# Performance work log

Measured on AMD Instinct MI355X. Metric: run time of the kernel, lower is better.

## Reference

```python
import jax, jax.numpy as jnp
import numpy as np

EMBED = 1024
HEADS = 16
HEAD_DIM = EMBED // HEADS
NUM_BUCKETS = 32
MAX_DISTANCE = 128
B, L = 4, 2048


def relative_position_bucket(relative_position, num_buckets=NUM_BUCKETS, max_distance=MAX_DISTANCE):
    # Faithful port of the torch helper (unidirectional T5 bucketing).
    n = -relative_position                       # [L, L] int32
    max_exact = num_buckets // 2
    is_small = n < max_exact
    nf = jnp.maximum(n, 1).astype(jnp.float32)   # guard log(<=0); masked out by is_small
    val_if_large = max_exact + (
        jnp.log(nf / max_exact) / np.log(max_distance / max_exact) * (num_buckets - max_exact)
    ).astype(jnp.int32)                          # .long() in torch truncates; values >=0 here
    val_if_large = jnp.minimum(val_if_large, num_buckets - 1)
    ret = jnp.where(is_small, n, val_if_large)
    return jnp.maximum(ret, 0)


def setup_inputs() -> dict:
    key = jax.random.key(0)
    ks = jax.random.split(key, 11)
    s = 0.02
    return {
        "x": jax.random.normal(ks[0], (B, L, EMBED), dtype=jnp.float32),
        "wq": jax.random.normal(ks[1], (EMBED, EMBED), dtype=jnp.float32) * s,
        "bq": jnp.zeros((EMBED,), dtype=jnp.float32),
        "wk": jax.random.normal(ks[2], (EMBED, EMBED), dtype=jnp.float32) * s,
        "bk": jnp.zeros((EMBED,), dtype=jnp.float32),
        "wv": jax.random.normal(ks[3], (EMBED, EMBED), dtype=jnp.float32) * s,
        "bv": jnp.zeros((EMBED,), dtype=jnp.float32),
        "wo": jax.random.normal(ks[4], (EMBED, EMBED), dtype=jnp.float32) * s,
        "bo": jnp.zeros((EMBED,), dtype=jnp.float32),
        "rel_bias": jax.random.normal(ks[5], (NUM_BUCKETS, HEADS), dtype=jnp.float32) * s,
    }


def reference(x, wq, bq, wk, bk, wv, bv, wo, bo, rel_bias):
    Bx, Lx, C = x.shape
    # torch nn.Linear: y = x @ W.T + b
    def proj(w, b):
        y = jnp.einsum("blc,dc->bld", x, w) + b
        return y.reshape(Bx, Lx, HEADS, HEAD_DIM).transpose(0, 2, 1, 3)  # [B,H,L,Dh]
    q = proj(wq, bq)
    k = proj(wk, bk)
    v = proj(wv, bv)
    scores = jnp.einsum("bhqd,bhkd->bhqk", q, k) / np.sqrt(HEAD_DIM)  # [B,H,L,L]
    ctx = jnp.arange(Lx, dtype=jnp.int32)
    relative = ctx[None, :] - ctx[:, None]                            # [L,L]
    bucket_ids = relative_position_bucket(relative)                   # [L,L]
    bias = rel_bias[bucket_ids]                                       # [L,L,H]
    bias = jnp.transpose(bias, (2, 0, 1))                             # [H,L,L]
    attn = jax.nn.softmax(scores + bias[None], axis=-1)
    out = jnp.einsum("bhqk,bhkd->bhqd", attn, v)                      # [B,H,L,Dh]
    out = out.transpose(0, 2, 1, 3).reshape(Bx, Lx, C)
    return jnp.einsum("blc,dc->bld", out, wo) + bo
```

## Files before the change

kernel.cpp:

```cpp
#include <hip/hip_runtime.h>

typedef __bf16 bf16x8 __attribute__((ext_vector_type(8)));
typedef __bf16 bf16x2 __attribute__((ext_vector_type(2)));
typedef float f32x4 __attribute__((ext_vector_type(4)));
typedef float f32x16 __attribute__((ext_vector_type(16)));
typedef short short8v __attribute__((ext_vector_type(8)));
typedef unsigned uint4v __attribute__((ext_vector_type(4)));
typedef unsigned short ushort_t;

#define EMB 1024
#define HEADS 16
#define HDIM 64
#define BATCH 4
#define SEQ 2048
#define LOG2E 1.44269504088896340736f
#define FIXED_M 12.0f

__device__ __forceinline__ ushort_t f2bf(float f) {
  union { float f; unsigned u; } x; x.f = f;
  unsigned r = x.u + 0x7fffu + ((x.u >> 16) & 1u);
  return (ushort_t)(r >> 16);
}

__device__ __forceinline__ unsigned pack2(float lo, float hi) {
  bf16x2 t;
  t.x = (__bf16)lo;
  t.y = (__bf16)hi;
  return __builtin_bit_cast(unsigned, t);
}

__device__ __forceinline__ void gload_lds16(const void* g, void* l) {
  __builtin_amdgcn_global_load_lds(
      (const __attribute__((address_space(1))) void*)g,
      (__attribute__((address_space(3))) void*)l, 16, 0, 0);
}

__global__ __launch_bounds__(256) void convert_all(
    const float* __restrict__ x,
    const float* __restrict__ wq, const float* __restrict__ wk,
    const float* __restrict__ wv, const float* __restrict__ wo,
    ushort_t* __restrict__ xb, ushort_t* __restrict__ wqb,
    ushort_t* __restrict__ wkb, ushort_t* __restrict__ wvb,
    ushort_t* __restrict__ wob) {
  int cid = blockIdx.x * 256 + threadIdx.x;
  const float* src;
  ushort_t* dst;
  int off;
  if (cid < 1048576) {
    src = x; dst = xb; off = cid;
  } else {
    int r = cid - 1048576;
    int wi = r >> 17;
    off = r & 131071;
    src = wi == 0 ? wq : wi == 1 ? wk : wi == 2 ? wv : wo;
    dst = wi == 0 ? wqb : wi == 1 ? wkb : wi == 2 ? wvb : wob;
  }
  const float4* s4 = (const float4*)(src + (size_t)off * 8);
  float4 a = s4[0], b = s4[1];
  ushort_t tmp[8] = {f2bf(a.x), f2bf(a.y), f2bf(a.z), f2bf(a.w),
                     f2bf(b.x), f2bf(b.y), f2bf(b.z), f2bf(b.w)};
  *(short8v*)(dst + (size_t)off * 8) = *(const short8v*)tmp;
}

__global__ __launch_bounds__(256) void build_biasR(
    const float* __restrict__ rel_bias, float* __restrict__ biasR) {
  int fid = blockIdx.x * 256 + threadIdx.x;
  int hh = fid >> 12;
  int p = (fid >> 10) & 3;
  int j = fid & 1023;
#pragma unroll
  for (int e = 0; e < 4; ++e) {
    int r = 4 * j + p + e;
    int n = 2048 - r;
    int bucket;
    if (n < 16) {
      bucket = n > 0 ? n : 0;
    } else {
      float tt = logf((float)n * 0.0625f) * (16.0f / logf(8.0f));
      int v = 16 + (int)tt;
      bucket = v < 31 ? v : 31;
    }
    biasR[(size_t)fid * 4 + e] = rel_bias[bucket * HEADS + hh] * LOG2E - FIXED_M;
  }
}

__global__ __launch_bounds__(256) void gemm_qkv(
    const ushort_t* __restrict__ xb,
    const ushort_t* __restrict__ wqb, const ushort_t* __restrict__ wkb,
    const ushort_t* __restrict__ wvb,
    const float* __restrict__ bq, const float* __restrict__ bk,
    const float* __restrict__ bv,
    ushort_t* __restrict__ qb, ushort_t* __restrict__ kb,
    ushort_t* __restrict__ vtb) {
  const int wgid = blockIdx.x;
  const int xcd = wgid & 7;
  const int r0 = wgid >> 3;
  const int nb = r0 % 24;
  const int mb = (r0 / 24) * 8 + xcd;
  const int wsel = nb >> 3;
  const int nloc = (nb & 7) * 128;
  const ushort_t* W = wsel == 0 ? wqb : wsel == 1 ? wkb : wvb;
  const float* bias = wsel == 0 ? bq : wsel == 1 ? bk : bv;
  const float scale = wsel == 0 ? 0.125f * LOG2E : 1.0f;

  __shared__ ushort_t Al[128 * 64];
  __shared__ ushort_t Bl[128 * 64];
  const int tid = threadIdx.x, lane = tid & 63, wid = tid >> 6;
  const int wm = wid >> 1, wn = wid & 1;
  const int srow = lane >> 3;
  const int scol = (lane & 7) * 8;
  f32x4 acc[4][4] = {};

  for (int kt = 0; kt < EMB / 64; ++kt) {
    const int k0 = kt * 64;
#pragma unroll
    for (int i = 0; i < 4; ++i) {
      int c = i * 4 + wid;
      int row = c * 8 + srow;
      gload_lds16(xb + (size_t)(mb * 128 + row) * EMB + k0 + scol, &Al[c * 512]);
      gload_lds16(W + (size_t)(nloc + row) * EMB + k0 + scol, &Bl[c * 512]);
    }
    __syncthreads();
#pragma unroll
    for (int kk = 0; kk < 2; ++kk) {
      const int koff = kk * 32 + (lane >> 4) * 8;
      bf16x8 af[4], bfv[4];
#pragma unroll
      for (int m = 0; m < 4; ++m)
        af[m] = *(const bf16x8*)&Al[(wm * 64 + m * 16 + (lane & 15)) * 64 + koff];
#pragma unroll
      for (int n = 0; n < 4; ++n)
        bfv[n] = *(const bf16x8*)&Bl[(wn * 64 + n * 16 + (lane & 15)) * 64 + koff];
#pragma unroll
      for (int m = 0; m < 4; ++m)
#pragma unroll
        for (int n = 0; n < 4; ++n)
          acc[m][n] = __builtin_amdgcn_mfma_f32_16x16x32_bf16(af[m], bfv[n],
                                                              acc[m][n], 0, 0, 0);
    }
    __syncthreads();
  }

#pragma unroll
  for (int m = 0; m < 4; ++m)
#pragma unroll
    for (int n = 0; n < 4; ++n)
#pragma unroll
      for (int r = 0; r < 4; ++r) {
        int row = mb * 128 + wm * 64 + m * 16 + (lane >> 4) * 4 + r;
        int col = nloc + wn * 64 + n * 16 + (lane & 15);
        float v = (acc[m][n][r] + bias[col]) * scale;
        int b = row >> 11, l = row & 2047;
        int hh = col >> 6, d = col & 63;
        if (wsel == 2) {
          vtb[(((size_t)(b * HEADS + hh) * HDIM) + d) * SEQ + l] = f2bf(v);
        } else {
          ushort_t* outp = wsel == 0 ? qb : kb;
          outp[(((size_t)(b * HEADS + hh) * SEQ) + l) * HDIM + d] = f2bf(v);
        }
      }
}

__global__ __launch_bounds__(256) void gemm_out(
    const ushort_t* __restrict__ ctxb, const ushort_t* __restrict__ wob,
    const float* __restrict__ bo, float* __restrict__ out) {
  const int wgid = blockIdx.x;
  const int xcd = wgid & 7;
  const int r0 = wgid >> 3;
  const int nb = r0 & 7;
  const int mb = (r0 >> 3) * 8 + xcd;
  __shared__ ushort_t Al[128 * 64];
  __shared__ ushort_t Bl[128 * 64];
  const int tid = threadIdx.x, lane = tid & 63, wid = tid >> 6;
  const int wm = wid >> 1, wn = wid & 1;
  const int srow = lane >> 3;
  const int scol = (lane & 7) * 8;
  f32x4 acc[4][4] = {};

  for (int kt = 0; kt < EMB / 64; ++kt) {
    const int k0 = kt * 64;
#pragma unroll
    for (int i = 0; i < 4; ++i) {
      int c = i * 4 + wid;
      int row = c * 8 + srow;
      gload_lds16(ctxb + (size_t)(mb * 128 + row) * EMB + k0 + scol, &Al[c * 512]);
      gload_lds16(wob + (size_t)(nb * 128 + row) * EMB + k0 + scol, &Bl[c * 512]);
    }
    __syncthreads();
#pragma unroll
    for (int kk = 0; kk < 2; ++kk) {
      const int koff = kk * 32 + (lane >> 4) * 8;
      bf16x8 af[4], bfv[4];
#pragma unroll
      for (int m = 0; m < 4; ++m)
        af[m] = *(const bf16x8*)&Al[(wm * 64 + m * 16 + (lane & 15)) * 64 + koff];
#pragma unroll
      for (int n = 0; n < 4; ++n)
        bfv[n] = *(const bf16x8*)&Bl[(wn * 64 + n * 16 + (lane & 15)) * 64 + koff];
#pragma unroll
      for (int m = 0; m < 4; ++m)
#pragma unroll
        for (int n = 0; n < 4; ++n)
          acc[m][n] = __builtin_amdgcn_mfma_f32_16x16x32_bf16(af[m], bfv[n],
                                                              acc[m][n], 0, 0, 0);
    }
    __syncthreads();
  }

#pragma unroll
  for (int m = 0; m < 4; ++m)
#pragma unroll
    for (int n = 0; n < 4; ++n)
#pragma unroll
      for (int r = 0; r < 4; ++r) {
        int row = mb * 128 + wm * 64 + m * 16 + (lane >> 4) * 4 + r;
        int col = nb * 128 + wn * 64 + n * 16 + (lane & 15);
        out[(size_t)row * EMB + col] = acc[m][n][r] + bo[col];
      }
}

__global__ __launch_bounds__(256) void attn(
    const ushort_t* __restrict__ qb, const ushort_t* __restrict__ kb,
    const ushort_t* __restrict__ vtb, const float* __restrict__ biasR,
    ushort_t* __restrict__ ctxb) {
  const int wgid = blockIdx.x;
  const int xcd = wgid & 7;
  const int sidx = wgid >> 3;
  const int qblk = sidx & 15;
  const int bh = ((sidx >> 4) << 3) | xcd;
  const int h = bh & 15, b = bh >> 4;
  const int tid = threadIdx.x;
  const int lane = tid & 63, w = tid >> 6;
  const int l31 = lane & 31, hi5 = lane >> 5;
  const int pidx = (lane ^ 32) << 2;

  __shared__ ushort_t SM[16384];

  const size_t base = (size_t)bh * (SEQ * HDIM);
  const int q = qblk * 128 + w * 32 + l31;

  bf16x8 qf[4];
#pragma unroll
  for (int s = 0; s < 4; ++s)
    qf[s] = *(const bf16x8*)&qb[base + (size_t)q * HDIM + s * 16 + hi5 * 8];

  int koA[4];
#pragma unroll
  for (int s = 0; s < 4; ++s)
    koA[s] = (s * 16 + hi5 * 8) ^ ((l31 & 7) << 3);
  const int rb0 = l31 * 64;
  const int rb1 = rb0 + 2048;

  const int p = (4 - (q & 3)) & 3;
  const int j00 = ((4 * hi5 - q + 2048) - p) >> 2;
  const float4* bptr = (const float4*)biasR + ((h * 4 + p) * 1024 + j00);

  const int chR0 = tid >> 3, chC0 = (tid & 7) * 8;
  const int chR1 = chR0 + 32;
  const int kd0 = chR0 * 64 + (chC0 ^ ((chR0 & 7) << 3));
  const int kd1 = chR1 * 64 + (chC0 ^ ((chR1 & 7) << 3));

  const ushort_t* kp0 = kb + base + (size_t)chR0 * HDIM + chC0;
  const ushort_t* kp1 = kb + base + (size_t)chR1 * HDIM + chC0;
  const ushort_t* vp0 = vtb + base + (size_t)chR0 * SEQ + chC0;
  const ushort_t* vp1 = vtb + base + (size_t)chR1 * SEQ + chC0;

  short8v kr0 = *(const short8v*)kp0;
  short8v kr1 = *(const short8v*)kp1;
  short8v vr0 = *(const short8v*)vp0;
  short8v vr1 = *(const short8v*)vp1;
  *(short8v*)&SM[kd0] = kr0;
  *(short8v*)&SM[kd1] = kr1;
  *(short8v*)&SM[4096 + kd0] = vr0;
  *(short8v*)&SM[4096 + kd1] = vr1;
  kp0 += 64 * HDIM; kp1 += 64 * HDIM; vp0 += 64; vp1 += 64;
  kr0 = *(const short8v*)kp0;
  kr1 = *(const short8v*)kp1;
  vr0 = *(const short8v*)vp0;
  vr1 = *(const short8v*)vp1;
  __syncthreads();

  f32x16 o0 = {}, o1 = {}, lv = {};

#pragma unroll 2
  for (int t = 0; t < 32; ++t) {
    const int c = t & 1;
    ushort_t* Kl = SM + c * 8192;
    ushort_t* Vl = Kl + 4096;

    float4 bw[8];
#pragma unroll
    for (int hh = 0; hh < 2; ++hh)
#pragma unroll
      for (int g = 0; g < 4; ++g)
        bw[hh * 4 + g] = bptr[hh * 8 + g * 2];

    f32x16 s0 = {}, s1 = {};
    __builtin_amdgcn_s_setprio(1);
#pragma unroll
    for (int s = 0; s < 4; ++s) {
      bf16x8 ka = *(const bf16x8*)&Kl[rb0 + koA[s]];
      s0 = __builtin_amdgcn_mfma_f32_32x32x16_bf16(ka, qf[s], s0, 0, 0, 0);
    }
#pragma unroll
    for (int s = 0; s < 4; ++s) {
      bf16x8 ka = *(const bf16x8*)&Kl[rb1 + koA[s]];
      s1 = __builtin_amdgcn_mfma_f32_32x32x16_bf16(ka, qf[s], s1, 0, 0, 0);
    }
    __builtin_amdgcn_s_setprio(0);

    if (t < 31) {
      ushort_t* Kn = SM + (c ^ 1) * 8192;
      *(short8v*)&Kn[kd0] = kr0;
      *(short8v*)&Kn[kd1] = kr1;
      *(short8v*)&Kn[4096 + kd0] = vr0;
      *(short8v*)&Kn[4096 + kd1] = vr1;
      kp0 += 64 * HDIM; kp1 += 64 * HDIM; vp0 += 64; vp1 += 64;
      kr0 = *(const short8v*)kp0;
      kr1 = *(const short8v*)kp1;
      vr0 = *(const short8v*)vp0;
      vr1 = *(const short8v*)vp1;
    }

#pragma unroll
    for (int r = 0; r < 16; ++r) {
      s0[r] += bw[r >> 2][r & 3];
      s1[r] += bw[4 + (r >> 2)][r & 3];
    }
#pragma unroll
    for (int r = 0; r < 16; ++r) s0[r] = __builtin_amdgcn_exp2f(s0[r]);
#pragma unroll
    for (int r = 0; r < 16; ++r) s1[r] = __builtin_amdgcn_exp2f(s1[r]);
    lv += s0;
    lv += s1;

    unsigned pk0[8], pk1[8];
#pragma unroll
    for (int d = 0; d < 8; ++d) {
      pk0[d] = pack2(s0[2 * d], s0[2 * d + 1]);
      pk1[d] = pack2(s1[2 * d], s1[2 * d + 1]);
    }
#pragma unroll
    for (int gsel = 0; gsel < 4; ++gsel) {
      int a = (gsel & 1) + (gsel >> 1) * 4;
      int bqi = a + 2;
      {
        unsigned tmp = hi5 ? pk0[a] : pk0[bqi];
        unsigned got = (unsigned)__builtin_amdgcn_ds_bpermute(pidx, (int)tmp);
        pk0[bqi] = hi5 ? pk0[bqi] : got;
        pk0[a] = hi5 ? got : pk0[a];
      }
      {
        unsigned tmp = hi5 ? pk1[a] : pk1[bqi];
        unsigned got = (unsigned)__builtin_amdgcn_ds_bpermute(pidx, (int)tmp);
        pk1[bqi] = hi5 ? pk1[bqi] : got;
        pk1[a] = hi5 ? got : pk1[a];
      }
    }

    bf16x8 paf[4];
    {
      uint4v t0 = {pk0[0], pk0[1], pk0[2], pk0[3]};
      uint4v t1 = {pk0[4], pk0[5], pk0[6], pk0[7]};
      uint4v t2 = {pk1[0], pk1[1], pk1[2], pk1[3]};
      uint4v t3 = {pk1[4], pk1[5], pk1[6], pk1[7]};
      paf[0] = __builtin_bit_cast(bf16x8, t0);
      paf[1] = __builtin_bit_cast(bf16x8, t1);
      paf[2] = __builtin_bit_cast(bf16x8, t2);
      paf[3] = __builtin_bit_cast(bf16x8, t3);
    }

    __builtin_amdgcn_s_setprio(1);
#pragma unroll
    for (int ss = 0; ss < 4; ++ss) {
      bf16x8 vb0 = *(const bf16x8*)&Vl[rb0 + koA[ss]];
      bf16x8 vb1 = *(const bf16x8*)&Vl[rb1 + koA[ss]];
      o0 = __builtin_amdgcn_mfma_f32_32x32x16_bf16(paf[ss], vb0, o0, 0, 0, 0);
      o1 = __builtin_amdgcn_mfma_f32_32x32x16_bf16(paf[ss], vb1, o1, 0, 0, 0);
    }
    __builtin_amdgcn_s_setprio(0);

    if (t < 31) __syncthreads();
    bptr += 16;
  }

  float li = (((lv[0] + lv[1]) + (lv[2] + lv[3])) +
              ((lv[4] + lv[5]) + (lv[6] + lv[7]))) +
             (((lv[8] + lv[9]) + (lv[10] + lv[11])) +
              ((lv[12] + lv[13]) + (lv[14] + lv[15])));
  float li2 = __int_as_float(
      __builtin_amdgcn_ds_bpermute(pidx, __float_as_int(li)));
  li += li2;
  float inv = 1.0f / li;
#pragma unroll
  for (int r = 0; r < 16; ++r) {
    int qr = (r & 3) + 8 * (r >> 2) + 4 * hi5;
    float iv = __int_as_float(
        __builtin_amdgcn_ds_bpermute(qr << 2, __float_as_int(inv)));
    o0[r] *= iv;
    o1[r] *= iv;
  }
  ushort_t* T = SM + w * 2048;
#pragma unroll
  for (int r = 0; r < 16; ++r) {
    int qr = (r & 3) + 8 * (r >> 2) + 4 * hi5;
    int sw = (qr & 7) << 3;
    T[qr * 64 + (l31 ^ sw)] = f2bf(o0[r]);
    T[qr * 64 + ((32 + l31) ^ sw)] = f2bf(o1[r]);
  }
  const int qr2 = lane >> 1;
  const int dh0 = (lane & 1) * 32;
  const int sw2 = (qr2 & 7) << 3;
  const size_t crow =
      ((size_t)b * SEQ + qblk * 128 + w * 32 + qr2) * EMB + h * 64;
#pragma unroll
  for (int c = 0; c < 4; ++c) {
    short8v vv = *(const short8v*)&T[qr2 * 64 + ((dh0 + c * 8) ^ sw2)];
    *(short8v*)&ctxb[crow + dh0 + c * 8] = vv;
  }
}

extern "C" void kernel_launch(void* const* d_in, const int* in_sizes, int n_in,
                              void* d_out, int out_size, void* d_ws, size_t ws_size,
                              hipStream_t stream) {
  const float* x = (const float*)d_in[0];
  const float* wq = (const float*)d_in[1];
  const float* bq = (const float*)d_in[2];
  const float* wk = (const float*)d_in[3];
  const float* bk = (const float*)d_in[4];
  const float* wv = (const float*)d_in[5];
  const float* bv = (const float*)d_in[6];
  const float* wo = (const float*)d_in[7];
  const float* bo = (const float*)d_in[8];
  const float* rel_bias = (const float*)d_in[9];
  float* out = (float*)d_out;

  char* ws = (char*)d_ws;
  ushort_t* xb  = (ushort_t*)(ws);
  ushort_t* wqb = (ushort_t*)(ws + 16777216);
  ushort_t* wkb = (ushort_t*)(ws + 16777216 + 2097152);
  ushort_t* wvb = (ushort_t*)(ws + 16777216 + 2 * 2097152);
  ushort_t* wob = (ushort_t*)(ws + 16777216 + 3 * 2097152);
  ushort_t* qb  = (ushort_t*)(ws + 25165824);
  ushort_t* kb  = (ushort_t*)(ws + 25165824 + 16777216);
  ushort_t* vtb = (ushort_t*)(ws + 25165824 + 2 * 16777216);
  float* biasR  = (float*)(ws + 75497472);
  ushort_t* ctxb = xb;

  convert_all<<<6144, 256, 0, stream>>>(x, wq, wk, wv, wo, xb, wqb, wkb, wvb, wob);
  build_biasR<<<256, 256, 0, stream>>>(rel_bias, biasR);
  gemm_qkv<<<1536, 256, 0, stream>>>(xb, wqb, wkb, wvb, bq, bk, bv, qb, kb, vtb);
  attn<<<1024, 256, 0, stream>>>(qb, kb, vtb, biasR, ctxb);
  gemm_out<<<512, 256, 0, stream>>>(ctxb, wob, bo, out);
}
```

Before: 283.7 us.

## Read K directly from global and stream V into LDS with direct loads

The attention kernel now uses 128-thread blocks covering 64 queries each, launched as 2048 blocks with a launch-bounds occupancy hint. K fragments are loaded straight from global memory into registers instead of being staged through shared memory. V tiles are double-buffered in LDS via direct global-to-LDS loads, synchronised by a single raw barrier plus a vmcnt wait. This removes the register-staged K/V copies and half the LDS footprint, at the cost of redundant per-wave K reads from cache and fragile hand-tuned wait counts.

```diff
diff --git a/kernel.cpp b/kernel.cpp
--- a/kernel.cpp
+++ b/kernel.cpp
@@ -219,30 +219,47 @@
       }
 }
 
-__global__ __launch_bounds__(256) void attn(
+__global__ __launch_bounds__(128, 4) void attn(
     const ushort_t* __restrict__ qb, const ushort_t* __restrict__ kb,
     const ushort_t* __restrict__ vtb, const float* __restrict__ biasR,
     ushort_t* __restrict__ ctxb) {
   const int wgid = blockIdx.x;
   const int xcd = wgid & 7;
   const int sidx = wgid >> 3;
-  const int qblk = sidx & 15;
-  const int bh = ((sidx >> 4) << 3) | xcd;
+  const int qblk = sidx & 31;
+  const int bh = ((sidx >> 5) << 3) | xcd;
   const int h = bh & 15, b = bh >> 4;
   const int tid = threadIdx.x;
   const int lane = tid & 63, w = tid >> 6;
   const int l31 = lane & 31, hi5 = lane >> 5;
   const int pidx = (lane ^ 32) << 2;
 
-  __shared__ ushort_t SM[16384];
+  __shared__ ushort_t SM[8192];
 
   const size_t base = (size_t)bh * (SEQ * HDIM);
-  const int q = qblk * 128 + w * 32 + l31;
+  const int q0 = qblk * 64 + w * 32;
+  const int q = q0 + l31;
 
   bf16x8 qf[4];
 #pragma unroll
   for (int s = 0; s < 4; ++s)
     qf[s] = *(const bf16x8*)&qb[base + (size_t)q * HDIM + s * 16 + hi5 * 8];
+
+  const ushort_t* kpA = kb + base + (size_t)l31 * HDIM + hi5 * 8;
+  const ushort_t* kpB = kpA + 32 * HDIM;
+
+  const int p = (4 - (q & 3)) & 3;
+  const int j00 = ((4 * hi5 - q + 2048) - p) >> 2;
+  const float4* bptr = (const float4*)biasR + ((h * 4 + p) * 1024 + j00);
+
+  const int vrow = w * 32 + (lane >> 3);
+  const ushort_t* vsrc =
+      vtb + base + (size_t)vrow * SEQ + ((lane & 7) ^ (lane >> 3)) * 8;
+  const int vdst = (w * 32) * 64;
+
+#pragma unroll
+  for (int i = 0; i < 4; ++i)
+    gload_lds16(vsrc + (size_t)i * 8 * SEQ, SM + vdst + i * 512);
 
   int koA[4];
 #pragma unroll
@@ -251,43 +268,9 @@
   const int rb0 = l31 * 64;
   const int rb1 = rb0 + 2048;
 
-  const int p = (4 - (q & 3)) & 3;
-  const int j00 = ((4 * hi5 - q + 2048) - p) >> 2;
-  const float4* bptr = (const float4*)biasR + ((h * 4 + p) * 1024 + j00);
-
-  const int chR0 = tid >> 3, chC0 = (tid & 7) * 8;
-  const int chR1 = chR0 + 32;
-  const int kd0 = chR0 * 64 + (chC0 ^ ((chR0 & 7) << 3));
-  const int kd1 = chR1 * 64 + (chC0 ^ ((chR1 & 7) << 3));
-
-  const ushort_t* kp0 = kb + base + (size_t)chR0 * HDIM + chC0;
-  const ushort_t* kp1 = kb + base + (size_t)chR1 * HDIM + chC0;
-  const ushort_t* vp0 = vtb + base + (size_t)chR0 * SEQ + chC0;
-  const ushort_t* vp1 = vtb + base + (size_t)chR1 * SEQ + chC0;
-
-  short8v kr0 = *(const short8v*)kp0;
-  short8v kr1 = *(const short8v*)kp1;
-  short8v vr0 = *(const short8v*)vp0;
-  short8v vr1 = *(const short8v*)vp1;
-  *(short8v*)&SM[kd0] = kr0;
-  *(short8v*)&SM[kd1] = kr1;
-  *(short8v*)&SM[4096 + kd0] = vr0;
-  *(short8v*)&SM[4096 + kd1] = vr1;
-  kp0 += 64 * HDIM; kp1 += 64 * HDIM; vp0 += 64; vp1 += 64;
-  kr0 = *(const short8v*)kp0;
-  kr1 = *(const short8v*)kp1;
-  vr0 = *(const short8v*)vp0;
-  vr1 = *(const short8v*)vp1;
-  __syncthreads();
-
   f32x16 o0 = {}, o1 = {}, lv = {};
 
-#pragma unroll 2
   for (int t = 0; t < 32; ++t) {
-    const int c = t & 1;
-    ushort_t* Kl = SM + c * 8192;
-    ushort_t* Vl = Kl + 4096;
-
     float4 bw[8];
 #pragma unroll
     for (int hh = 0; hh < 2; ++hh)
@@ -299,28 +282,17 @@
     __builtin_amdgcn_s_setprio(1);
 #pragma unroll
     for (int s = 0; s < 4; ++s) {
-      bf16x8 ka = *(const bf16x8*)&Kl[rb0 + koA[s]];
+      bf16x8 ka = *(const bf16x8*)(kpA + s * 16);
       s0 = __builtin_amdgcn_mfma_f32_32x32x16_bf16(ka, qf[s], s0, 0, 0, 0);
     }
 #pragma unroll
     for (int s = 0; s < 4; ++s) {
-      bf16x8 ka = *(const bf16x8*)&Kl[rb1 + koA[s]];
-      s1 = __builtin_amdgcn_mfma_f32_32x32x16_bf16(ka, qf[s], s1, 0, 0, 0);
+      bf16x8 kbv = *(const bf16x8*)(kpB + s * 16);
+      s1 = __builtin_amdgcn_mfma_f32_32x32x16_bf16(kbv, qf[s], s1, 0, 0, 0);
     }
     __builtin_amdgcn_s_setprio(0);
-
-    if (t < 31) {
-      ushort_t* Kn = SM + (c ^ 1) * 8192;
-      *(short8v*)&Kn[kd0] = kr0;
-      *(short8v*)&Kn[kd1] = kr1;
-      *(short8v*)&Kn[4096 + kd0] = vr0;
-      *(short8v*)&Kn[4096 + kd1] = vr1;
-      kp0 += 64 * HDIM; kp1 += 64 * HDIM; vp0 += 64; vp1 += 64;
-      kr0 = *(const short8v*)kp0;
-      kr1 = *(const short8v*)kp1;
-      vr0 = *(const short8v*)vp0;
-      vr1 = *(const short8v*)vp1;
-    }
+    kpA += 64 * HDIM;
+    kpB += 64 * HDIM;
 
 #pragma unroll
     for (int r = 0; r < 16; ++r) {
@@ -370,6 +342,19 @@
       paf[3] = __builtin_bit_cast(bf16x8, t3);
     }
 
+    __builtin_amdgcn_s_barrier();
+    __builtin_amdgcn_sched_barrier(0);
+    asm volatile("s_waitcnt vmcnt(8)" ::: "memory");
+
+    ushort_t* Vl = SM + (t & 1) * 4096;
+    if (t < 31) {
+      ushort_t* Vn = SM + ((t + 1) & 1) * 4096;
+#pragma unroll
+      for (int i = 0; i < 4; ++i)
+        gload_lds16(vsrc + (size_t)(t + 1) * 64 + (size_t)i * 8 * SEQ,
+                    Vn + vdst + i * 512);
+    }
+
     __builtin_amdgcn_s_setprio(1);
 #pragma unroll
     for (int ss = 0; ss < 4; ++ss) {
@@ -379,8 +364,6 @@
       o1 = __builtin_amdgcn_mfma_f32_32x32x16_bf16(paf[ss], vb1, o1, 0, 0, 0);
     }
     __builtin_amdgcn_s_setprio(0);
-
-    if (t < 31) __syncthreads();
     bptr += 16;
   }
 
@@ -411,8 +394,7 @@
   const int qr2 = lane >> 1;
   const int dh0 = (lane & 1) * 32;
   const int sw2 = (qr2 & 7) << 3;
-  const size_t crow =
-      ((size_t)b * SEQ + qblk * 128 + w * 32 + qr2) * EMB + h * 64;
+  const size_t crow = ((size_t)b * SEQ + q0 + qr2) * EMB + h * 64;
 #pragma unroll
   for (int c = 0; c < 4; ++c) {
     short8v vv = *(const short8v*)&T[qr2 * 64 + ((dh0 + c * 8) ^ sw2)];
@@ -450,6 +432,6 @@
   convert_all<<<6144, 256, 0, stream>>>(x, wq, wk, wv, wo, xb, wqb, wkb, wvb, wob);
   build_biasR<<<256, 256, 0, stream>>>(rel_bias, biasR);
   gemm_qkv<<<1536, 256, 0, stream>>>(xb, wqb, wkb, wvb, bq, bk, bv, qb, kb, vtb);
-  attn<<<1024, 256, 0, stream>>>(qb, kb, vtb, biasR, ctxb);
+  attn<<<2048, 128, 0, stream>>>(qb, kb, vtb, biasR, ctxb);
   gemm_out<<<512, 256, 0, stream>>>(ctxb, wob, bo, out);
 }
```

Measured after the change: 455.2 us. +60.5%, slower.
